# Optimization experiments

Hardware: AMD Instinct MI355X
Metric: run time of the kernel (lower is better)

Reference implementation:

```python
import jax, jax.numpy as jnp
import numpy as np

B = 8          # graphs (FOVs)
NPG = 16384    # clusters per graph
N = B * NPG
K = 6          # knn k=5+1, loop=True
E = N * K
C0PG = 2048    # superclusters_0 per graph
C0 = B * C0PG
C1PG = 256     # superclusters_1 per graph
C1 = B * C1PG
L = 10         # 4 cluster-level + 3 SC0 + 3 SC1 PointTransformerConv layers
D = 64


def setup_inputs() -> dict:
    key = jax.random.key(0)
    ks = jax.random.split(key, 20)
    s = 0.05  # weight scale for stable attention logits
    x = jax.random.normal(ks[0], (N, D), jnp.float32)
    pos_c = jax.random.uniform(ks[1], (N, 2), jnp.float32)
    dst_c = jnp.repeat(jnp.arange(N, dtype=jnp.int32), K)
    src_c = jax.random.randint(ks[2], (E,), 0, N, jnp.int32)
    src_c = src_c.at[::K].set(jnp.arange(N, dtype=jnp.int32))  # self-loops
    batch = (jnp.arange(N, dtype=jnp.int32) // NPG)
    sc_id0 = (jnp.arange(N, dtype=jnp.int32) % C0PG)   # every SC0 id present per graph
    pos_sc0 = jax.random.uniform(ks[3], (C0, 2), jnp.float32)
    sc_id1 = (jnp.arange(C0, dtype=jnp.int32) % C1PG)
    pos_sc1 = jax.random.uniform(ks[4], (C1, 2), jnp.float32)
    return dict(
        x=x, pos_c=pos_c, src_c=src_c, dst_c=dst_c, batch=batch,
        sc_id0=sc_id0, pos_sc0=pos_sc0, sc_id1=sc_id1, pos_sc1=pos_sc1,
        Wlin=jax.random.normal(ks[5], (L, D, D)) * s,
        Wsrc=jax.random.normal(ks[6], (L, D, D)) * s,
        Wdst=jax.random.normal(ks[7], (L, D, D)) * s,
        pW1=jax.random.normal(ks[8], (L, 2, D)) * s,
        pB1=jnp.zeros((L, D), jnp.float32),
        pW2=jax.random.normal(ks[9], (L, D, D)) * s,
        pB2=jnp.zeros((L, D), jnp.float32),
        aW1=jax.random.normal(ks[10], (L, D, D)) * s,
        aB1=jnp.zeros((L, D), jnp.float32),
        aW2=jax.random.normal(ks[11], (L, D, D)) * s,
        aB2=jnp.zeros((L, D), jnp.float32),
        head_w=jax.random.normal(ks[12], (D, 2)) * s,
        head_b=jnp.zeros((2,), jnp.float32),
    )


def mlp2(x, W1, b1, W2, b2):
    # PyG MLP(plain_last=False): Linear->ReLU twice (eval mode, BN at init = identity)
    h = jax.nn.relu(x @ W1 + b1)
    return jax.nn.relu(h @ W2 + b2)


def ptconv(h, pos, src, dst, n, p, l):
    # PointTransformerConv: delta = pos_nn(pos_i - pos_j);
    # alpha = softmax_i(attn_nn(lin_dst(x)_i - lin_src(x)_j + delta));
    # out_i = max_j alpha * (lin(x)_j + delta)
    xv = h @ p['Wlin'][l]
    a_src = h @ p['Wsrc'][l]
    a_dst = h @ p['Wdst'][l]
    delta = mlp2(pos[dst] - pos[src], p['pW1'][l], p['pB1'][l], p['pW2'][l], p['pB2'][l])
    a = mlp2(a_dst[dst] - a_src[src] + delta, p['aW1'][l], p['aB1'][l], p['aW2'][l], p['aB2'][l])
    m = jax.ops.segment_max(a, dst, num_segments=n)
    e = jnp.exp(a - m[dst])
    ssum = jax.ops.segment_sum(e, dst, num_segments=n)
    alpha = e / ssum[dst]
    return jax.ops.segment_max(alpha * (xv[src] + delta), dst, num_segments=n)


def gen_cluster(ids, batch, nb):
    mx = jax.ops.segment_max(ids, batch, num_segments=nb)
    off = jnp.cumsum(jnp.concatenate([jnp.zeros((1,), ids.dtype), mx + 1]))
    return ids + off[batch].astype(ids.dtype)


def knn_edges(pos, b, npg, k):
    # knn_graph(k, loop=True) per graph: src=neighbor, dst=center
    p = pos.reshape(b, npg, 2)
    sq = jnp.sum(p * p, axis=-1)
    d2 = sq[:, :, None] + sq[:, None, :] - 2.0 * jnp.einsum('bnd,bmd->bnm', p, p)
    idx = jax.lax.top_k(-d2, k)[1]  # [b, npg, k], includes self (d=0)
    src = (idx + (jnp.arange(b) * npg)[:, None, None]).reshape(-1).astype(jnp.int32)
    dst = jnp.repeat(jnp.arange(b * npg, dtype=jnp.int32), k)
    return src, dst


def reference(x, pos_c, src_c, dst_c, batch, sc_id0, pos_sc0, sc_id1, pos_sc1,
              Wlin, Wsrc, Wdst, pW1, pB1, pW2, pB2, aW1, aB1, aW2, aB2,
              head_w, head_b):
    p = dict(Wlin=Wlin, Wsrc=Wsrc, Wdst=Wdst, pW1=pW1, pB1=pB1, pW2=pW2, pB2=pB2,
             aW1=aW1, aB1=aB1, aW2=aW2, aB2=aB2)
    h = x
    for l in range(4):  # cluster_encoder_0..3 on clusters graph
        h = ptconv(h, pos_c, src_c, dst_c, N, p, l)
    # pool clusters -> superclusters_0
    cl0 = gen_cluster(sc_id0, batch, B)
    h0 = jax.ops.segment_max(h, cl0, num_segments=C0)
    batch0 = jax.ops.segment_max(batch, cl0, num_segments=C0)
    src0, dst0 = knn_edges(pos_sc0, B, C0PG, K)
    for l in range(4, 7):
        h0 = ptconv(h0, pos_sc0, src0, dst0, C0, p, l)
    # pool SC0 -> superclusters_1
    cl1 = gen_cluster(sc_id1, batch0, B)
    h1 = jax.ops.segment_max(h0, cl1, num_segments=C1)
    batch1 = jax.ops.segment_max(batch0, cl1, num_segments=C1)
    src1, dst1 = knn_edges(pos_sc1, B, C1PG, K)
    for l in range(7, 10):
        h1 = ptconv(h1, pos_sc1, src1, dst1, C1, p, l)
    g = jax.ops.segment_max(h1, batch1, num_segments=B)  # global_max_pool
    return g @ head_w + head_b
```

## Files before the change

kernel.cpp:

```cpp
#include <hip/hip_runtime.h>
#include <cstdint>

namespace {
constexpr int BG   = 8;
constexpr int NPG  = 16384;
constexpr int NN   = BG * NPG;
constexpr int KK   = 6;
constexpr int C0PG = 2048;
constexpr int C0N  = BG * C0PG;
constexpr int C1PG = 256;
constexpr int C1N  = BG * C1PG;
constexpr int D    = 64;
constexpr int SEG0 = C0PG / 256;
constexpr int VS   = 198;
constexpr int NMS  = 132;
}

__device__ __forceinline__ unsigned f2u_ord(float v) {
  unsigned u = __float_as_uint(v);
  return (u & 0x80000000u) ? ~u : (u | 0x80000000u);
}

__global__ void k_init_u32(unsigned* __restrict__ p, unsigned v, int n) {
  int i = blockIdx.x * blockDim.x + threadIdx.x;
  if (i < n) p[i] = v;
}

__global__ void k_seg_max_i32(const int* __restrict__ vals, const int* __restrict__ seg,
                              int* __restrict__ out, int n) {
  int i = blockIdx.x * blockDim.x + threadIdx.x;
  if (i < n) atomicMax(&out[seg[i]], vals[i]);
}

template <int NB>
__global__ __launch_bounds__(256) void k_seg_max_small(
    const int* __restrict__ vals, const int* __restrict__ seg,
    int* __restrict__ out, int n) {
  __shared__ int lmx[NB];
  int t = threadIdx.x;
  if (t < NB) lmx[t] = (int)0x80000000;
  __syncthreads();
  for (int i = blockIdx.x * 256 + t; i < n; i += gridDim.x * 256)
    atomicMax(&lmx[seg[i]], vals[i]);
  __syncthreads();
  if (t < NB) atomicMax(&out[t], lmx[t]);
}

__global__ void k_cumsum_off(const int* __restrict__ mx, int* __restrict__ off, int nb) {
  if (threadIdx.x == 0 && blockIdx.x == 0) {
    int a = 0; off[0] = 0;
    for (int b = 0; b < nb; ++b) { a += mx[b] + 1; off[b + 1] = a; }
  }
}

__global__ void k_gen_cl(const int* __restrict__ ids, const int* __restrict__ bt,
                         const int* __restrict__ off, int* __restrict__ cl, int n) {
  int i = blockIdx.x * blockDim.x + threadIdx.x;
  if (i < n) cl[i] = ids[i] + off[bt[i]];
}

__global__ void k_pool_f32(const float* __restrict__ h, const int* __restrict__ cl,
                           unsigned* __restrict__ outu, int total) {
  int i = blockIdx.x * blockDim.x + threadIdx.x;
  if (i < total) atomicMax(&outu[(size_t)cl[i >> 6] * D + (i & 63)], f2u_ord(h[i]));
}

__global__ void k_decode_f32(unsigned* __restrict__ p, int n) {
  int i = blockIdx.x * blockDim.x + threadIdx.x;
  if (i < n) { unsigned u = p[i]; p[i] = (u & 0x80000000u) ? (u ^ 0x80000000u) : ~u; }
}

__global__ __launch_bounds__(256) void k_knn(const float* __restrict__ pos, int npg,
                                             int* __restrict__ srcOut) {
  #pragma clang fp contract(off)
  __shared__ float px[2048], py[2048], sq[2048];
  int t = threadIdx.x;
  int nglob = blockIdx.x * 256 + t;
  int graph = nglob / npg;
  int base = graph * npg;
  for (int i = t; i < npg; i += 256) {
    float xx = pos[2 * (base + i)];
    float yy = pos[2 * (base + i) + 1];
    px[i] = xx; py[i] = yy;
    float a = xx * xx; float b = yy * yy;
    sq[i] = a + b;
  }
  __syncthreads();
  int i = nglob - base;
  float xi = px[i], yi = py[i], sqi = sq[i];
  float bd[KK]; int bi[KK];
  #pragma unroll
  for (int q = 0; q < KK; ++q) { bd[q] = 3.4e38f; bi[q] = 0; }
  for (int j = 0; j < npg; ++j) {
    float t1 = xi * px[j];
    float t2 = yi * py[j];
    float dot = t1 + t2;
    float d2 = (sqi + sq[j]) - 2.0f * dot;
    if (d2 < bd[KK - 1]) {
      bd[KK - 1] = d2; bi[KK - 1] = j;
      #pragma unroll
      for (int q = KK - 1; q > 0; --q) {
        if (bd[q] < bd[q - 1]) {
          float td = bd[q]; bd[q] = bd[q - 1]; bd[q - 1] = td;
          int ti = bi[q]; bi[q] = bi[q - 1]; bi[q - 1] = ti;
        }
      }
    }
  }
  #pragma unroll
  for (int q = 0; q < KK; ++q) srcOut[(size_t)nglob * KK + q] = base + bi[q];
}

__global__ __launch_bounds__(256) void k_knn_part(const float* __restrict__ pos, int npg,
                                                  int nseg,
                                                  float* __restrict__ outD,
                                                  int* __restrict__ outI) {
  #pragma clang fp contract(off)
  __shared__ float cx[256], cy[256], cs[256];
  int t = threadIdx.x;
  int qt = blockIdx.x / nseg;
  int s  = blockIdx.x % nseg;
  int qlo = qt * 256;
  int graph = qlo / npg;
  int base = graph * npg;
  int cbase = base + s * 256;
  {
    float xx = pos[2 * (cbase + t)];
    float yy = pos[2 * (cbase + t) + 1];
    cx[t] = xx; cy[t] = yy;
    float a = xx * xx; float b = yy * yy;
    cs[t] = a + b;
  }
  __syncthreads();
  int q = qlo + t;
  float xi = pos[2 * q], yi = pos[2 * q + 1];
  float qa = xi * xi; float qb = yi * yi;
  float sqi = qa + qb;
  float bd[KK]; int bi[KK];
  #pragma unroll
  for (int u = 0; u < KK; ++u) { bd[u] = 3.4e38f; bi[u] = 0; }
  for (int j = 0; j < 256; ++j) {
    float t1 = xi * cx[j];
    float t2 = yi * cy[j];
    float dot = t1 + t2;
    float d2 = (sqi + cs[j]) - 2.0f * dot;
    if (d2 < bd[KK - 1]) {
      bd[KK - 1] = d2; bi[KK - 1] = cbase + j;
      #pragma unroll
      for (int u = KK - 1; u > 0; --u) {
        if (bd[u] < bd[u - 1]) {
          float td = bd[u]; bd[u] = bd[u - 1]; bd[u - 1] = td;
          int ti = bi[u]; bi[u] = bi[u - 1]; bi[u - 1] = ti;
        }
      }
    }
  }
  size_t ob = (size_t)q * (nseg * KK) + (size_t)s * KK;
  #pragma unroll
  for (int u = 0; u < KK; ++u) { outD[ob + u] = bd[u]; outI[ob + u] = bi[u]; }
}

__global__ void k_knn_merge(const float* __restrict__ inD, const int* __restrict__ inI,
                            int nseg, int* __restrict__ srcOut, int nq) {
  int q = blockIdx.x * blockDim.x + threadIdx.x;
  if (q >= nq) return;
  float bd[KK]; int bi[KK];
  #pragma unroll
  for (int u = 0; u < KK; ++u) { bd[u] = 3.4e38f; bi[u] = 0x7fffffff; }
  size_t ib = (size_t)q * (nseg * KK);
  for (int e = 0; e < nseg * KK; ++e) {
    float d = inD[ib + e]; int ix = inI[ib + e];
    bool lt = (d < bd[KK - 1]) || (d == bd[KK - 1] && ix < bi[KK - 1]);
    if (lt) {
      bd[KK - 1] = d; bi[KK - 1] = ix;
      #pragma unroll
      for (int u = KK - 1; u > 0; --u) {
        bool sw = (bd[u] < bd[u - 1]) || (bd[u] == bd[u - 1] && bi[u] < bi[u - 1]);
        if (sw) {
          float td = bd[u]; bd[u] = bd[u - 1]; bd[u - 1] = td;
          int ti = bi[u]; bi[u] = bi[u - 1]; bi[u - 1] = ti;
        }
      }
    }
  }
  #pragma unroll
  for (int u = 0; u < KK; ++u) srcOut[(size_t)q * KK + u] = bi[u];
}

__global__ void __launch_bounds__(256)
__attribute__((amdgpu_waves_per_eu(4, 4)))
k_node_mm(const float* __restrict__ hin,
    const float* __restrict__ Wl, const float* __restrict__ Ws, const float* __restrict__ Wd,
    float* __restrict__ xv, float* __restrict__ as_, float* __restrict__ ad_) {
  __shared__ float wbuf[2048];
  __shared__ float vbuf[32 * NMS];
  int t = threadIdx.x;
  size_t nb = (size_t)blockIdx.x * 128;
  int ng = t >> 3, cb = t & 7, c0 = cb * 8;
  const float* Wm[3] = {Wl, Ws, Wd};
  float* Om[3] = {xv, as_, ad_};
  const float4* h4 = (const float4*)hin;
  float acc[3][32];
  #pragma unroll
  for (int m = 0; m < 3; ++m)
    #pragma unroll
    for (int i = 0; i < 32; ++i) acc[m][i] = 0.0f;
  for (int kh = 0; kh < 2; ++kh) {
    #pragma unroll
    for (int r = 0; r < 4; ++r) {
      int flat = r * 256 + t;
      int n = flat >> 3, kq = flat & 7;
      float4 hv = h4[(nb + n) * 16 + kh * 8 + kq];
      vbuf[(kq * 4 + 0) * NMS + n] = hv.x;
      vbuf[(kq * 4 + 1) * NMS + n] = hv.y;
      vbuf[(kq * 4 + 2) * NMS + n] = hv.z;
      vbuf[(kq * 4 + 3) * NMS + n] = hv.w;
    }
    #pragma unroll
    for (int m = 0; m < 3; ++m) {
      {
        const float4* w4 = (const float4*)Wm[m] + kh * 512;
        float4* wb = (float4*)wbuf;
        wb[t] = w4[t];
        wb[256 + t] = w4[256 + t];
      }
      __syncthreads();
      #pragma clang loop unroll_count(2)
      for (int kk = 0; kk < 32; ++kk) {
        float4 v4 = *(const float4*)&vbuf[kk * NMS + 4 * ng];
        float4 w0 = *(const float4*)&wbuf[kk * 64 + c0];
        float4 w1 = *(const float4*)&wbuf[kk * 64 + c0 + 4];
        float vv[4] = {v4.x, v4.y, v4.z, v4.w};
        float wv[8] = {w0.x, w0.y, w0.z, w0.w, w1.x, w1.y, w1.z, w1.w};
        #pragma unroll
        for (int ni = 0; ni < 4; ++ni)
          #pragma unroll
          for (int c = 0; c < 8; ++c)
            acc[m][ni * 8 + c] = fmaf(vv[ni], wv[c], acc[m][ni * 8 + c]);
      }
      __syncthreads();
    }
  }
  #pragma unroll
  for (int m = 0; m < 3; ++m) {
    float* O = Om[m];
    #pragma unroll
    for (int ni = 0; ni < 4; ++ni) {
      *(float4*)(O + (nb + 4 * ng + ni) * 64 + c0) =
          make_float4(acc[m][ni * 8 + 0], acc[m][ni * 8 + 1],
                      acc[m][ni * 8 + 2], acc[m][ni * 8 + 3]);
      *(float4*)(O + (nb + 4 * ng + ni) * 64 + c0 + 4) =
          make_float4(acc[m][ni * 8 + 4], acc[m][ni * 8 + 5],
                      acc[m][ni * 8 + 6], acc[m][ni * 8 + 7]);
    }
  }
}

__global__ void __launch_bounds__(256)
__attribute__((amdgpu_waves_per_eu(3, 3)))
k_edge_fused(
    const float* __restrict__ pos, const int* __restrict__ srcA,
    const float* __restrict__ as_, const float* __restrict__ ad_,
    const float* __restrict__ xv,
    const float* __restrict__ pW1, const float* __restrict__ pB1,
    const float* __restrict__ pW2, const float* __restrict__ pB2,
    const float* __restrict__ aW1, const float* __restrict__ aB1,
    const float* __restrict__ aW2, const float* __restrict__ aB2,
    float* __restrict__ hout) {
  __shared__ float wbuf[2048];
  __shared__ float vbuf[32 * VS];
  __shared__ float sbuf[192];
  __shared__ float pdxs[192], pdys[192];
  __shared__ int   srcb[192];
  int t = threadIdx.x;
  int nb = blockIdx.x * 32;
  int ng = t >> 3;
  int cb = t & 7;
  int cl = 4 * cb;
  int ch = 32 + 4 * cb;
  int node = nb + ng;

  if (t < 192) {
    int s = srcA[(size_t)nb * KK + t];
    srcb[t] = s;
    int dn = nb + t / KK;
    float2 pd = *(const float2*)(pos + 2 * (size_t)dn);
    float2 ps = *(const float2*)(pos + 2 * (size_t)s);
    pdxs[t] = pd.x - ps.x;
    pdys[t] = pd.y - ps.y;
    sbuf[t] = (t < 128) ? pW1[t] : pB1[t - 128];
  }
  __syncthreads();

  float d[48];
  {
    float4 b0 = *(const float4*)(pB2 + cl);
    float4 b1 = *(const float4*)(pB2 + ch);
    #pragma unroll
    for (int j = 0; j < 6; ++j) {
      d[j * 8 + 0] = b0.x; d[j * 8 + 1] = b0.y; d[j * 8 + 2] = b0.z; d[j * 8 + 3] = b0.w;
      d[j * 8 + 4] = b1.x; d[j * 8 + 5] = b1.y; d[j * 8 + 6] = b1.z; d[j * 8 + 7] = b1.w;
    }
  }
  #pragma unroll
  for (int h = 0; h < 2; ++h) {
    {
      const float4* w4 = (const float4*)pW2 + h * 512;
      float4* wb = (float4*)wbuf;
      wb[t] = w4[t];
      wb[256 + t] = w4[256 + t];
    }
    if (t < 192) {
      float px = pdxs[t], py = pdys[t];
      #pragma clang loop unroll_count(4)
      for (int kk = 0; kk < 32; ++kk) {
        int k = h * 32 + kk;
        float p0 = px * sbuf[k];
        float p1 = py * sbuf[64 + k];
        float ph = fmaxf((p0 + p1) + sbuf[128 + k], 0.0f);
        vbuf[kk * VS + t] = ph;
      }
    }
    __syncthreads();
    #pragma clang loop unroll_count(2)
    for (int kk = 0; kk < 32; ++kk) {
      float2 v01 = *(const float2*)&vbuf[kk * VS + 6 * ng];
      float2 v23 = *(const float2*)&vbuf[kk * VS + 6 * ng + 2];
      float2 v45 = *(const float2*)&vbuf[kk * VS + 6 * ng + 4];
      float4 w0 = *(const float4*)&wbuf[kk * 64 + cl];
      float4 w1 = *(const float4*)&wbuf[kk * 64 + ch];
      float vv[6] = {v01.x, v01.y, v23.x, v23.y, v45.x, v45.y};
      float wv[8] = {w0.x, w0.y, w0.z, w0.w, w1.x, w1.y, w1.z, w1.w};
      #pragma unroll
      for (int j = 0; j < 6; ++j)
        #pragma unroll
        for (int c = 0; c < 8; ++c)
          d[j * 8 + c] = fmaf(vv[j], wv[c], d[j * 8 + c]);
    }
    __syncthreads();
  }
  #pragma unroll
  for (int i = 0; i < 48; ++i) d[i] = fmaxf(d[i], 0.0f);

  float r[48];
  {
    float4 b0 = *(const float4*)(aB1 + cl);
    float4 b1 = *(const float4*)(aB1 + ch);
    #pragma unroll
    for (int j = 0; j < 6; ++j) {
      r[j * 8 + 0] = b0.x; r[j * 8 + 1] = b0.y; r[j * 8 + 2] = b0.z; r[j * 8 + 3] = b0.w;
      r[j * 8 + 4] = b1.x; r[j * 8 + 5] = b1.y; r[j * 8 + 6] = b1.z; r[j * 8 + 7] = b1.w;
    }
  }
  #pragma unroll
  for (int h = 0; h < 2; ++h) {
    {
      const float4* w4 = (const float4*)aW1 + h * 512;
      float4* wb = (float4*)wbuf;
      wb[t] = w4[t];
      wb[256 + t] = w4[256 + t];
    }
    {
      int cbase = h ? ch : cl;
      float4 av = *(const float4*)(ad_ + (size_t)node * 64 + cbase);
      float vtmp[6][4];
      #pragma unroll
      for (int j = 0; j < 6; ++j) {
        int s = srcb[6 * ng + j];
        float4 sv = *(const float4*)(as_ + (size_t)s * 64 + cbase);
        vtmp[j][0] = (av.x - sv.x) + d[j * 8 + 4 * h + 0];
        vtmp[j][1] = (av.y - sv.y) + d[j * 8 + 4 * h + 1];
        vtmp[j][2] = (av.z - sv.z) + d[j * 8 + 4 * h + 2];
        vtmp[j][3] = (av.w - sv.w) + d[j * 8 + 4 * h + 3];
      }
      #pragma unroll
      for (int cj = 0; cj < 4; ++cj)
        #pragma unroll
        for (int jp = 0; jp < 3; ++jp)
          *(float2*)&vbuf[(4 * cb + cj) * VS + 6 * ng + 2 * jp] =
              make_float2(vtmp[2 * jp][cj], vtmp[2 * jp + 1][cj]);
    }
    __syncthreads();
    #pragma clang loop unroll_count(2)
    for (int kk = 0; kk < 32; ++kk) {
      float2 v01 = *(const float2*)&vbuf[kk * VS + 6 * ng];
      float2 v23 = *(const float2*)&vbuf[kk * VS + 6 * ng + 2];
      float2 v45 = *(const float2*)&vbuf[kk * VS + 6 * ng + 4];
      float4 w0 = *(const float4*)&wbuf[kk * 64 + cl];
      float4 w1 = *(const float4*)&wbuf[kk * 64 + ch];
      float vv[6] = {v01.x, v01.y, v23.x, v23.y, v45.x, v45.y};
      float wv[8] = {w0.x, w0.y, w0.z, w0.w, w1.x, w1.y, w1.z, w1.w};
      #pragma unroll
      for (int j = 0; j < 6; ++j)
        #pragma unroll
        for (int c = 0; c < 8; ++c)
          r[j * 8 + c] = fmaf(vv[j], wv[c], r[j * 8 + c]);
    }
    __syncthreads();
  }
  #pragma unroll
  for (int i = 0; i < 48; ++i) r[i] = fmaxf(r[i], 0.0f);

  float a[48];
  {
    float4 b0 = *(const float4*)(aB2 + cl);
    float4 b1 = *(const float4*)(aB2 + ch);
    #pragma unroll
    for (int j = 0; j < 6; ++j) {
      a[j * 8 + 0] = b0.x; a[j * 8 + 1] = b0.y; a[j * 8 + 2] = b0.z; a[j * 8 + 3] = b0.w;
      a[j * 8 + 4] = b1.x; a[j * 8 + 5] = b1.y; a[j * 8 + 6] = b1.z; a[j * 8 + 7] = b1.w;
    }
  }
  #pragma unroll
  for (int h = 0; h < 2; ++h) {
    {
      const float4* w4 = (const float4*)aW2 + h * 512;
      float4* wb = (float4*)wbuf;
      wb[t] = w4[t];
      wb[256 + t] = w4[256 + t];
    }
    #pragma unroll
    for (int cj = 0; cj < 4; ++cj)
      #pragma unroll
      for (int jp = 0; jp < 3; ++jp)
        *(float2*)&vbuf[(4 * cb + cj) * VS + 6 * ng + 2 * jp] =
            make_float2(r[(2 * jp) * 8 + 4 * h + cj], r[(2 * jp + 1) * 8 + 4 * h + cj]);
    __syncthreads();
    #pragma clang loop unroll_count(2)
    for (int kk = 0; kk < 32; ++kk) {
      float2 v01 = *(const float2*)&vbuf[kk * VS + 6 * ng];
      float2 v23 = *(const float2*)&vbuf[kk * VS + 6 * ng + 2];
      float2 v45 = *(const float2*)&vbuf[kk * VS + 6 * ng + 4];
      float4 w0 = *(const float4*)&wbuf[kk * 64 + cl];
      float4 w1 = *(const float4*)&wbuf[kk * 64 + ch];
      float vv[6] = {v01.x, v01.y, v23.x, v23.y, v45.x, v45.y};
      float wv[8] = {w0.x, w0.y, w0.z, w0.w, w1.x, w1.y, w1.z, w1.w};
      #pragma unroll
      for (int j = 0; j < 6; ++j)
        #pragma unroll
        for (int c = 0; c < 8; ++c)
          a[j * 8 + c] = fmaf(vv[j], wv[c], a[j * 8 + c]);
    }
    __syncthreads();
  }
  #pragma unroll
  for (int i = 0; i < 48; ++i) a[i] = fmaxf(a[i], 0.0f);

  float m8[8], ss[8], out[8];
  #pragma unroll
  for (int c = 0; c < 8; ++c) m8[c] = a[c];
  #pragma unroll
  for (int j = 1; j < 6; ++j)
    #pragma unroll
    for (int c = 0; c < 8; ++c) m8[c] = fmaxf(m8[c], a[j * 8 + c]);
  #pragma unroll
  for (int c = 0; c < 8; ++c) ss[c] = 0.0f;
  #pragma unroll
  for (int j = 0; j < 6; ++j)
    #pragma unroll
    for (int c = 0; c < 8; ++c) ss[c] += expf(a[j * 8 + c] - m8[c]);
  #pragma unroll
  for (int j = 0; j < 6; ++j) {
    int s = srcb[6 * ng + j];
    float4 x0 = *(const float4*)(xv + (size_t)s * 64 + cl);
    float4 x1 = *(const float4*)(xv + (size_t)s * 64 + ch);
    float xa[8] = {x0.x, x0.y, x0.z, x0.w, x1.x, x1.y, x1.z, x1.w};
    #pragma unroll
    for (int c = 0; c < 8; ++c) {
      float ej = expf(a[j * 8 + c] - m8[c]);
      float alpha = ej / ss[c];
      float val = alpha * (xa[c] + d[j * 8 + c]);
      out[c] = (j == 0) ? val : fmaxf(out[c], val);
    }
  }
  *(float4*)(hout + (size_t)node * 64 + cl) = make_float4(out[0], out[1], out[2], out[3]);
  *(float4*)(hout + (size_t)node * 64 + ch) = make_float4(out[4], out[5], out[6], out[7]);
}

__global__ void k_head(const float* __restrict__ g, const float* __restrict__ hw,
                       const float* __restrict__ hb, float* __restrict__ out) {
  int t = threadIdx.x;
  if (t >= BG * 2) return;
  int b = t >> 1, o = t & 1;
  float acc = 0.0f;
  for (int k = 0; k < D; ++k) acc = fmaf(g[b * D + k], hw[k * 2 + o], acc);
  out[b * 2 + o] = acc + hb[o];
}

extern "C" void kernel_launch(void* const* d_in, const int* in_sizes, int n_in,
                              void* d_out, int out_size, void* d_ws, size_t ws_size,
                              hipStream_t stream) {
  (void)in_sizes; (void)n_in; (void)out_size; (void)ws_size;
  const float* x      = (const float*)d_in[0];
  const float* pos_c  = (const float*)d_in[1];
  const int*   src_c  = (const int*)d_in[2];
  const int*   batch  = (const int*)d_in[4];
  const int*   sc_id0 = (const int*)d_in[5];
  const float* pos_s0 = (const float*)d_in[6];
  const int*   sc_id1 = (const int*)d_in[7];
  const float* pos_s1 = (const float*)d_in[8];
  const float* Wlin = (const float*)d_in[9];
  const float* Wsrc = (const float*)d_in[10];
  const float* Wdst = (const float*)d_in[11];
  const float* pW1  = (const float*)d_in[12];
  const float* pB1  = (const float*)d_in[13];
  const float* pW2  = (const float*)d_in[14];
  const float* pB2  = (const float*)d_in[15];
  const float* aW1  = (const float*)d_in[16];
  const float* aB1  = (const float*)d_in[17];
  const float* aW2  = (const float*)d_in[18];
  const float* aB2  = (const float*)d_in[19];
  const float* hw   = (const float*)d_in[20];
  const float* hb   = (const float*)d_in[21];
  float* outp = (float*)d_out;

  char* ws = (char*)d_ws;
  size_t off = 0;
  auto alloc = [&](size_t bytes) -> void* {
    void* p = ws + off; off = (off + bytes + 255) & ~(size_t)255; return p;
  };
  float* h   = (float*)alloc((size_t)NN * D * 4);
  float* xv  = (float*)alloc((size_t)NN * D * 4);
  float* as_ = (float*)alloc((size_t)NN * D * 4);
  float* ad_ = (float*)alloc((size_t)NN * D * 4);
  float* h0  = (float*)alloc((size_t)C0N * D * 4);
  float* h1  = (float*)alloc((size_t)C1N * D * 4);
  float* g   = (float*)alloc((size_t)BG * D * 4);
  int* cl0   = (int*)alloc((size_t)NN * 4);
  int* cl1   = (int*)alloc((size_t)C0N * 4);
  int* b0    = (int*)alloc((size_t)C0N * 4);
  int* b1    = (int*)alloc((size_t)C1N * 4);
  int* src0  = (int*)alloc((size_t)C0N * KK * 4);
  int* src1  = (int*)alloc((size_t)C1N * KK * 4);
  float* kd  = (float*)alloc((size_t)C0N * SEG0 * KK * 4);
  int*   ki  = (int*)alloc((size_t)C0N * SEG0 * KK * 4);
  int* mx    = (int*)alloc(256);
  int* offb  = (int*)alloc(256);

  auto ptconv = [&](int n, const float* pos, const int* srcA,
                    const float* hin, float* hout, int l) {
    k_node_mm<<<n / 128, 256, 0, stream>>>(hin,
        Wlin + (size_t)l * 4096, Wsrc + (size_t)l * 4096, Wdst + (size_t)l * 4096,
        xv, as_, ad_);
    k_edge_fused<<<n / 32, 256, 0, stream>>>(pos, srcA, as_, ad_, xv,
        pW1 + (size_t)l * 128, pB1 + (size_t)l * 64,
        pW2 + (size_t)l * 4096, pB2 + (size_t)l * 64,
        aW1 + (size_t)l * 4096, aB1 + (size_t)l * 64,
        aW2 + (size_t)l * 4096, aB2 + (size_t)l * 64,
        hout);
  };

  k_init_u32<<<1, 64, 0, stream>>>((unsigned*)mx, 0x80000000u, BG);
  k_seg_max_small<BG><<<64, 256, 0, stream>>>(sc_id0, batch, mx, NN);
  k_cumsum_off<<<1, 1, 0, stream>>>(mx, offb, BG);
  k_gen_cl<<<NN / 256, 256, 0, stream>>>(sc_id0, batch, offb, cl0, NN);
  k_init_u32<<<(C0N + 255) / 256, 256, 0, stream>>>((unsigned*)b0, 0x80000000u, C0N);
  k_seg_max_i32<<<NN / 256, 256, 0, stream>>>(batch, cl0, b0, NN);
  k_knn_part<<<(C0N / 256) * SEG0, 256, 0, stream>>>(pos_s0, C0PG, SEG0, kd, ki);
  k_knn_merge<<<C0N / 256, 256, 0, stream>>>(kd, ki, SEG0, src0, C0N);
  k_init_u32<<<1, 64, 0, stream>>>((unsigned*)mx, 0x80000000u, BG);
  k_seg_max_small<BG><<<64, 256, 0, stream>>>(sc_id1, b0, mx, C0N);
  k_cumsum_off<<<1, 1, 0, stream>>>(mx, offb, BG);
  k_gen_cl<<<C0N / 256, 256, 0, stream>>>(sc_id1, b0, offb, cl1, C0N);
  k_init_u32<<<(C1N + 255) / 256, 256, 0, stream>>>((unsigned*)b1, 0x80000000u, C1N);
  k_seg_max_i32<<<C0N / 256, 256, 0, stream>>>(b0, cl1, b1, C0N);
  k_knn<<<C1N / 256, 256, 0, stream>>>(pos_s1, C1PG, src1);

  ptconv(NN, pos_c, src_c, x, h, 0);
  for (int l = 1; l < 4; ++l) ptconv(NN, pos_c, src_c, h, h, l);
  k_init_u32<<<C0N * D / 256, 256, 0, stream>>>((unsigned*)h0, 0x007fffffu, C0N * D);
  k_pool_f32<<<NN * D / 256, 256, 0, stream>>>(h, cl0, (unsigned*)h0, NN * D);
  k_decode_f32<<<C0N * D / 256, 256, 0, stream>>>((unsigned*)h0, C0N * D);
  for (int l = 4; l < 7; ++l) ptconv(C0N, pos_s0, src0, h0, h0, l);
  k_init_u32<<<C1N * D / 256, 256, 0, stream>>>((unsigned*)h1, 0x007fffffu, C1N * D);
  k_pool_f32<<<C0N * D / 256, 256, 0, stream>>>(h0, cl1, (unsigned*)h1, C0N * D);
  k_decode_f32<<<C1N * D / 256, 256, 0, stream>>>((unsigned*)h1, C1N * D);
  for (int l = 7; l < 10; ++l) ptconv(C1N, pos_s1, src1, h1, h1, l);
  k_init_u32<<<(BG * D + 255) / 256, 256, 0, stream>>>((unsigned*)g, 0x007fffffu, BG * D);
  k_pool_f32<<<C1N * D / 256, 256, 0, stream>>>(h1, b1, (unsigned*)g, C1N * D);
  k_decode_f32<<<(BG * D + 255) / 256, 256, 0, stream>>>((unsigned*)g, BG * D);
  k_head<<<1, 64, 0, stream>>>(g, hw, hb, outp);
}
```

Measured before the change: 1.901 ms.

## Double-buffer MLP weights and make edge staging wave-local to drop barriers

The weight tile buffer in the fused edge kernel becomes double-buffered, so the next 32x64 weight slice is loaded while the current slice's GEMM runs. Edge staging is remapped so each wavefront produces exactly the 48 edges that its own threads later consume. That lets the barrier between staging and GEMM go away, roughly halving the block-wide __syncthreads per layer. The cost is 8 KB more LDS per block and reliance on intra-wave ordering of LDS accesses for correctness.

```diff
diff --git a/kernel.cpp b/kernel.cpp
--- a/kernel.cpp
+++ b/kernel.cpp
@@ -267,7 +267,7 @@
     const float* __restrict__ aW1, const float* __restrict__ aB1,
     const float* __restrict__ aW2, const float* __restrict__ aB2,
     float* __restrict__ hout) {
-  __shared__ float wbuf[2048];
+  __shared__ float wbuf[2][2048];
   __shared__ float vbuf[32 * VS];
   __shared__ float sbuf[192];
   __shared__ float pdxs[192], pdys[192];
@@ -279,170 +279,152 @@
   int cl = 4 * cb;
   int ch = 32 + 4 * cb;
   int node = nb + ng;
-
-  if (t < 192) {
-    int s = srcA[(size_t)nb * KK + t];
-    srcb[t] = s;
-    int dn = nb + t / KK;
+  int wv_ = t >> 6, ln = t & 63;
+  int eidx = 48 * wv_ + ln;
+  bool stg = (ln < 48);
+
+  float d[48], r[48], a[48];
+
+  if (t < 192) sbuf[t] = (t < 128) ? pW1[t] : pB1[t - 128];
+  if (stg) {
+    int s = srcA[(size_t)nb * KK + eidx];
+    srcb[eidx] = s;
+    int dn = nb + eidx / 6;
     float2 pd = *(const float2*)(pos + 2 * (size_t)dn);
     float2 ps = *(const float2*)(pos + 2 * (size_t)s);
-    pdxs[t] = pd.x - ps.x;
-    pdys[t] = pd.y - ps.y;
-    sbuf[t] = (t < 128) ? pW1[t] : pB1[t - 128];
-  }
-  __syncthreads();
-
-  float d[48];
+    pdxs[eidx] = pd.x - ps.x;
+    pdys[eidx] = pd.y - ps.y;
+  }
   {
-    float4 b0 = *(const float4*)(pB2 + cl);
-    float4 b1 = *(const float4*)(pB2 + ch);
-    #pragma unroll
-    for (int j = 0; j < 6; ++j) {
-      d[j * 8 + 0] = b0.x; d[j * 8 + 1] = b0.y; d[j * 8 + 2] = b0.z; d[j * 8 + 3] = b0.w;
-      d[j * 8 + 4] = b1.x; d[j * 8 + 5] = b1.y; d[j * 8 + 6] = b1.z; d[j * 8 + 7] = b1.w;
-    }
-  }
-  #pragma unroll
-  for (int h = 0; h < 2; ++h) {
-    {
-      const float4* w4 = (const float4*)pW2 + h * 512;
-      float4* wb = (float4*)wbuf;
-      wb[t] = w4[t];
-      wb[256 + t] = w4[256 + t];
-    }
-    if (t < 192) {
-      float px = pdxs[t], py = pdys[t];
+    const float4* w4 = (const float4*)pW2;
+    float4* wb = (float4*)wbuf[0];
+    wb[t] = w4[t];
+    wb[256 + t] = w4[256 + t];
+  }
+  __syncthreads();
+
+  auto loadW = [&](const float* W, int parity) {
+    const float4* w4 = (const float4*)W;
+    float4 x0 = w4[t];
+    float4 x1 = w4[256 + t];
+    float4* wb = (float4*)wbuf[parity];
+    wb[t] = x0;
+    wb[256 + t] = x1;
+  };
+  auto stage_ph = [&](int h) {
+    if (stg) {
+      float px = pdxs[eidx], py = pdys[eidx];
       #pragma clang loop unroll_count(4)
       for (int kk = 0; kk < 32; ++kk) {
         int k = h * 32 + kk;
         float p0 = px * sbuf[k];
         float p1 = py * sbuf[64 + k];
-        float ph = fmaxf((p0 + p1) + sbuf[128 + k], 0.0f);
-        vbuf[kk * VS + t] = ph;
+        vbuf[kk * VS + eidx] = fmaxf((p0 + p1) + sbuf[128 + k], 0.0f);
       }
     }
-    __syncthreads();
+  };
+  auto gemm = [&](float* acc, int parity) {
+    const float* wb = wbuf[parity];
     #pragma clang loop unroll_count(2)
     for (int kk = 0; kk < 32; ++kk) {
       float2 v01 = *(const float2*)&vbuf[kk * VS + 6 * ng];
       float2 v23 = *(const float2*)&vbuf[kk * VS + 6 * ng + 2];
       float2 v45 = *(const float2*)&vbuf[kk * VS + 6 * ng + 4];
-      float4 w0 = *(const float4*)&wbuf[kk * 64 + cl];
-      float4 w1 = *(const float4*)&wbuf[kk * 64 + ch];
+      float4 w0 = *(const float4*)&wb[kk * 64 + cl];
+      float4 w1 = *(const float4*)&wb[kk * 64 + ch];
       float vv[6] = {v01.x, v01.y, v23.x, v23.y, v45.x, v45.y};
       float wv[8] = {w0.x, w0.y, w0.z, w0.w, w1.x, w1.y, w1.z, w1.w};
       #pragma unroll
       for (int j = 0; j < 6; ++j)
         #pragma unroll
         for (int c = 0; c < 8; ++c)
-          d[j * 8 + c] = fmaf(vv[j], wv[c], d[j * 8 + c]);
-    }
-    __syncthreads();
-  }
-  #pragma unroll
-  for (int i = 0; i < 48; ++i) d[i] = fmaxf(d[i], 0.0f);
-
-  float r[48];
-  {
-    float4 b0 = *(const float4*)(aB1 + cl);
-    float4 b1 = *(const float4*)(aB1 + ch);
+          acc[j * 8 + c] = fmaf(vv[j], wv[c], acc[j * 8 + c]);
+    }
+  };
+  auto stage_v = [&](int h) {
+    int cbase = h ? ch : cl;
+    float4 av = *(const float4*)(ad_ + (size_t)node * 64 + cbase);
+    float vtmp[6][4];
     #pragma unroll
     for (int j = 0; j < 6; ++j) {
-      r[j * 8 + 0] = b0.x; r[j * 8 + 1] = b0.y; r[j * 8 + 2] = b0.z; r[j * 8 + 3] = b0.w;
-      r[j * 8 + 4] = b1.x; r[j * 8 + 5] = b1.y; r[j * 8 + 6] = b1.z; r[j * 8 + 7] = b1.w;
-    }
-  }
-  #pragma unroll
-  for (int h = 0; h < 2; ++h) {
-    {
-      const float4* w4 = (const float4*)aW1 + h * 512;
-      float4* wb = (float4*)wbuf;
-      wb[t] = w4[t];
-      wb[256 + t] = w4[256 + t];
-    }
-    {
-      int cbase = h ? ch : cl;
-      float4 av = *(const float4*)(ad_ + (size_t)node * 64 + cbase);
-      float vtmp[6][4];
+      int s = srcb[6 * ng + j];
+      float4 sv = *(const float4*)(as_ + (size_t)s * 64 + cbase);
+      vtmp[j][0] = (av.x - sv.x) + d[j * 8 + 4 * h + 0];
+      vtmp[j][1] = (av.y - sv.y) + d[j * 8 + 4 * h + 1];
+      vtmp[j][2] = (av.z - sv.z) + d[j * 8 + 4 * h + 2];
+      vtmp[j][3] = (av.w - sv.w) + d[j * 8 + 4 * h + 3];
+    }
+    #pragma unroll
+    for (int cj = 0; cj < 4; ++cj)
       #pragma unroll
-      for (int j = 0; j < 6; ++j) {
-        int s = srcb[6 * ng + j];
-        float4 sv = *(const float4*)(as_ + (size_t)s * 64 + cbase);
-        vtmp[j][0] = (av.x - sv.x) + d[j * 8 + 4 * h + 0];
-        vtmp[j][1] = (av.y - sv.y) + d[j * 8 + 4 * h + 1];
-        vtmp[j][2] = (av.z - sv.z) + d[j * 8 + 4 * h + 2];
-        vtmp[j][3] = (av.w - sv.w) + d[j * 8 + 4 * h + 3];
-      }
-      #pragma unroll
-      for (int cj = 0; cj < 4; ++cj)
-        #pragma unroll
-        for (int jp = 0; jp < 3; ++jp)
-          *(float2*)&vbuf[(4 * cb + cj) * VS + 6 * ng + 2 * jp] =
-              make_float2(vtmp[2 * jp][cj], vtmp[2 * jp + 1][cj]);
-    }
-    __syncthreads();
-    #pragma clang loop unroll_count(2)
-    for (int kk = 0; kk < 32; ++kk) {
-      float2 v01 = *(const float2*)&vbuf[kk * VS + 6 * ng];
-      float2 v23 = *(const float2*)&vbuf[kk * VS + 6 * ng + 2];
-      float2 v45 = *(const float2*)&vbuf[kk * VS + 6 * ng + 4];
-      float4 w0 = *(const float4*)&wbuf[kk * 64 + cl];
-      float4 w1 = *(const float4*)&wbuf[kk * 64 + ch];
-      float vv[6] = {v01.x, v01.y, v23.x, v23.y, v45.x, v45.y};
-      float wv[8] = {w0.x, w0.y, w0.z, w0.w, w1.x, w1.y, w1.z, w1.w};
-      #pragma unroll
-      for (int j = 0; j < 6; ++j)
-        #pragma unroll
-        for (int c = 0; c < 8; ++c)
-          r[j * 8 + c] = fmaf(vv[j], wv[c], r[j * 8 + c]);
-    }
-    __syncthreads();
-  }
-  #pragma unroll
-  for (int i = 0; i < 48; ++i) r[i] = fmaxf(r[i], 0.0f);
-
-  float a[48];
-  {
-    float4 b0 = *(const float4*)(aB2 + cl);
-    float4 b1 = *(const float4*)(aB2 + ch);
-    #pragma unroll
-    for (int j = 0; j < 6; ++j) {
-      a[j * 8 + 0] = b0.x; a[j * 8 + 1] = b0.y; a[j * 8 + 2] = b0.z; a[j * 8 + 3] = b0.w;
-      a[j * 8 + 4] = b1.x; a[j * 8 + 5] = b1.y; a[j * 8 + 6] = b1.z; a[j * 8 + 7] = b1.w;
-    }
-  }
-  #pragma unroll
-  for (int h = 0; h < 2; ++h) {
-    {
-      const float4* w4 = (const float4*)aW2 + h * 512;
-      float4* wb = (float4*)wbuf;
-      wb[t] = w4[t];
-      wb[256 + t] = w4[256 + t];
-    }
+      for (int jp = 0; jp < 3; ++jp)
+        *(float2*)&vbuf[(4 * cb + cj) * VS + 6 * ng + 2 * jp] =
+            make_float2(vtmp[2 * jp][cj], vtmp[2 * jp + 1][cj]);
+  };
+  auto stage_r = [&](int h) {
     #pragma unroll
     for (int cj = 0; cj < 4; ++cj)
       #pragma unroll
       for (int jp = 0; jp < 3; ++jp)
         *(float2*)&vbuf[(4 * cb + cj) * VS + 6 * ng + 2 * jp] =
             make_float2(r[(2 * jp) * 8 + 4 * h + cj], r[(2 * jp + 1) * 8 + 4 * h + cj]);
-    __syncthreads();
-    #pragma clang loop unroll_count(2)
-    for (int kk = 0; kk < 32; ++kk) {
-      float2 v01 = *(const float2*)&vbuf[kk * VS + 6 * ng];
-      float2 v23 = *(const float2*)&vbuf[kk * VS + 6 * ng + 2];
-      float2 v45 = *(const float2*)&vbuf[kk * VS + 6 * ng + 4];
-      float4 w0 = *(const float4*)&wbuf[kk * 64 + cl];
-      float4 w1 = *(const float4*)&wbuf[kk * 64 + ch];
-      float vv[6] = {v01.x, v01.y, v23.x, v23.y, v45.x, v45.y};
-      float wv[8] = {w0.x, w0.y, w0.z, w0.w, w1.x, w1.y, w1.z, w1.w};
-      #pragma unroll
-      for (int j = 0; j < 6; ++j)
-        #pragma unroll
-        for (int c = 0; c < 8; ++c)
-          a[j * 8 + c] = fmaf(vv[j], wv[c], a[j * 8 + c]);
-    }
-    __syncthreads();
-  }
+  };
+
+  {
+    float4 b0 = *(const float4*)(pB2 + cl);
+    float4 b1 = *(const float4*)(pB2 + ch);
+    #pragma unroll
+    for (int j = 0; j < 6; ++j) {
+      d[j * 8 + 0] = b0.x; d[j * 8 + 1] = b0.y; d[j * 8 + 2] = b0.z; d[j * 8 + 3] = b0.w;
+      d[j * 8 + 4] = b1.x; d[j * 8 + 5] = b1.y; d[j * 8 + 6] = b1.z; d[j * 8 + 7] = b1.w;
+    }
+  }
+  stage_ph(0);
+  loadW(pW2 + 2048, 1);
+  gemm(d, 0);
+  __syncthreads();
+  stage_ph(1);
+  loadW(aW1, 0);
+  gemm(d, 1);
+  __syncthreads();
+  #pragma unroll
+  for (int i = 0; i < 48; ++i) d[i] = fmaxf(d[i], 0.0f);
+
+  {
+    float4 b0 = *(const float4*)(aB1 + cl);
+    float4 b1 = *(const float4*)(aB1 + ch);
+    #pragma unroll
+    for (int j = 0; j < 6; ++j) {
+      r[j * 8 + 0] = b0.x; r[j * 8 + 1] = b0.y; r[j * 8 + 2] = b0.z; r[j * 8 + 3] = b0.w;
+      r[j * 8 + 4] = b1.x; r[j * 8 + 5] = b1.y; r[j * 8 + 6] = b1.z; r[j * 8 + 7] = b1.w;
+    }
+  }
+  stage_v(0);
+  loadW(aW1 + 2048, 1);
+  gemm(r, 0);
+  __syncthreads();
+  stage_v(1);
+  loadW(aW2, 0);
+  gemm(r, 1);
+  __syncthreads();
+  #pragma unroll
+  for (int i = 0; i < 48; ++i) r[i] = fmaxf(r[i], 0.0f);
+
+  {
+    float4 b0 = *(const float4*)(aB2 + cl);
+    float4 b1 = *(const float4*)(aB2 + ch);
+    #pragma unroll
+    for (int j = 0; j < 6; ++j) {
+      a[j * 8 + 0] = b0.x; a[j * 8 + 1] = b0.y; a[j * 8 + 2] = b0.z; a[j * 8 + 3] = b0.w;
+      a[j * 8 + 4] = b1.x; a[j * 8 + 5] = b1.y; a[j * 8 + 6] = b1.z; a[j * 8 + 7] = b1.w;
+    }
+  }
+  stage_r(0);
+  loadW(aW2 + 2048, 1);
+  gemm(a, 0);
+  __syncthreads();
+  stage_r(1);
+  gemm(a, 1);
   #pragma unroll
   for (int i = 0; i < 48; ++i) a[i] = fmaxf(a[i], 0.0f);
 
```

Result: no change. 1.874 ms (-1.4%).
